# Optimization experiments

Measured on AMD Instinct MI355X. Metric: run time of the kernel, lower is better.

## Reference

```python
import jax, jax.numpy as jnp
import numpy as np

D = 20          # embedding dim (hardcoded in original module)
N_REL = 200     # relation vocab size (table has N_REL+1 rows)
N_TIME = 365    # time embedding table size
L = 3           # propagation layers
E = 2_000_000   # edges per layer
N = 1_000_000   # node-slot pool per layer
B = 64          # batch size
N_ENT = 1_000_003


def setup_inputs() -> dict:
    key = jax.random.key(0)
    ks = jax.random.split(key, 16)
    src_idx = jax.random.randint(ks[0], (L, E), 0, N, dtype=jnp.int32)
    dst_idx = jax.random.randint(ks[1], (L, E), 0, N, dtype=jnp.int32)
    rel_idx = jax.random.randint(ks[2], (L, E), 0, N_REL + 1, dtype=jnp.int32)
    qrel_idx = jax.random.randint(ks[3], (L, E), 0, N_REL + 1, dtype=jnp.int32)
    # signed relative time (edge_time - query_time); abs() must stay < N_TIME
    rel_time = jax.random.randint(ks[4], (L, E), -(N_TIME - 1), N_TIME, dtype=jnp.int32)
    node_batch = jax.random.randint(ks[5], (N,), 0, B, dtype=jnp.int32)
    node_ent = jnp.arange(N, dtype=jnp.int32)  # unique entity per final node slot
    s = 0.1
    rela_embed = jax.random.normal(ks[6], (N_REL + 1, D), jnp.float32) * s
    time_embed = jax.random.normal(ks[7], (N_TIME, D), jnp.float32) * s
    w_att1 = jax.random.normal(ks[8], (30, 3 * D), jnp.float32) * s
    w_att2 = jax.random.normal(ks[9], (1, 30), jnp.float32) * s
    w_past = jax.random.normal(ks[10], (D, D), jnp.float32) * s
    w_now = jax.random.normal(ks[11], (D, D), jnp.float32) * s
    w_future = jax.random.normal(ks[12], (D, D), jnp.float32) * s
    w_cls = jax.random.normal(ks[13], (D,), jnp.float32) * s
    b_cls = jnp.zeros((), jnp.float32)
    return dict(src_idx=src_idx, dst_idx=dst_idx, rel_idx=rel_idx,
                qrel_idx=qrel_idx, rel_time=rel_time, node_batch=node_batch,
                node_ent=node_ent, rela_embed=rela_embed, time_embed=time_embed,
                w_att1=w_att1, w_att2=w_att2, w_past=w_past, w_now=w_now,
                w_future=w_future, w_cls=w_cls, b_cls=b_cls,
                batch_size=B, n_ent=N_ENT)


def reference(src_idx, dst_idx, rel_idx, qrel_idx, rel_time, node_batch,
              node_ent, rela_embed, time_embed, w_att1, w_att2, w_past,
              w_now, w_future, w_cls, b_cls, batch_size, n_ent):
    n_layers = src_idx.shape[0]
    n_nodes = node_batch.shape[0]
    d = rela_embed.shape[1]
    hidden = jnp.zeros((n_nodes, d), dtype=rela_embed.dtype)
    for l in range(n_layers):
        rt = rel_time[l]                         # [E] signed relative time
        h_src = hidden[src_idx[l]]               # [E, D] gather
        r_emb = rela_embed[rel_idx[l]]           # [E, D]
        t_emb = time_embed[jnp.abs(rt)]          # [E, D]
        embed_rel = h_src + r_emb + t_emb
        # conditional time-branch MLP (mask-partitioned linear, same math as
        # the original's boolean-masked assignments)
        fut = embed_rel @ w_future.T
        now = embed_rel @ w_now.T
        pst = embed_rel @ w_past.T
        transformed = jnp.where((rt > 0)[:, None], fut,
                       jnp.where((rt == 0)[:, None], now, pst))
        # attention over concat(hidden_src, rel_emb, query_rel_emb)  [E, 3D]
        att_in = jnp.concatenate([h_src, r_emb, rela_embed[qrel_idx[l]]], axis=1)
        score = jax.nn.sigmoid(jax.nn.relu(att_in @ w_att1.T) @ w_att2.T)  # [E,1]
        msg = score * transformed                # [E, D]
        hidden = jax.ops.segment_sum(msg, dst_idx[l], num_segments=n_nodes)
        hidden = jax.nn.leaky_relu(hidden)       # default slope 0.01, as torch
    result = hidden @ w_cls + b_cls              # [N]
    score_all = jnp.zeros((batch_size, n_ent), dtype=result.dtype)
    score_all = score_all.at[node_batch, node_ent].set(result)
    return score_all
```

## Files before the change

kernel.cpp:

```cpp
#include <hip/hip_runtime.h>
#include <hip/hip_bf16.h>
#include <cstdint>

#define DD 20
#define HID 30
#define NB_SCAN 1024

typedef unsigned int  u32;
typedef unsigned short u16;

__device__ __forceinline__ void load20(const float* __restrict__ p, float* r){
  const float4* q = (const float4*)p;
#pragma unroll
  for (int i=0;i<5;i++){ float4 v=q[i]; r[4*i+0]=v.x; r[4*i+1]=v.y; r[4*i+2]=v.z; r[4*i+3]=v.w; }
}

__device__ __forceinline__ u32 pkbf(float a, float b){
  u32 ua=__float_as_uint(a); ua=(ua+0x7FFFu+((ua>>16)&1u))>>16;
  u32 ub=__float_as_uint(b); ub=(ub+0x7FFFu+((ub>>16)&1u))>>16;
  return ua | (ub<<16);
}

__global__ void k_prep(const float* __restrict__ rela, const float* __restrict__ w1,
                       const float* __restrict__ wp, const float* __restrict__ wn,
                       const float* __restrict__ wf,
                       float* __restrict__ W3, float* __restrict__ AR, float* __restrict__ AQ,
                       int nrel){
  int t = blockIdx.x*blockDim.x + threadIdx.x;
  if (t < 3*DD*DD){
    int s = t/(DD*DD), idx = t%(DD*DD);
    W3[t] = (s==0)?wp[idx]:((s==1)?wn[idx]:wf[idx]);
  }
  if (t < nrel*HID){
    int r=t/HID, j=t-r*HID;
    float sr=0.f, sq=0.f;
#pragma unroll
    for (int k=0;k<DD;k++){
      float e = rela[r*DD+k];
      sr += e*w1[j*3*DD + DD + k];
      sq += e*w1[j*3*DD + 2*DD + k];
    }
    AR[r*32+j]=sr; AQ[r*32+j]=sq;
  }
}

__global__ void k_rwtw(const float* __restrict__ rela, const float* __restrict__ timee,
                       const float* __restrict__ W3,
                       float* __restrict__ RW, float* __restrict__ TW,
                       int nrel, int ntime){
  int t = blockIdx.x*blockDim.x+threadIdx.x;
  int totR = 3*nrel*DD, totT = 3*ntime*DD;
  if (t < totR){
    int sel = t/(nrel*DD); int rem = t - sel*nrel*DD; int r = rem/DD; int i = rem - r*DD;
    const float* w = W3 + sel*DD*DD + i*DD;
    const float* e = rela + (size_t)r*DD;
    float s=0.f;
#pragma unroll
    for (int k=0;k<DD;k++) s += e[k]*w[k];
    RW[t]=s;
  }
  if (t < totT){
    int sel = t/(ntime*DD); int rem = t - sel*ntime*DD; int tt = rem/DD; int i = rem - tt*DD;
    const float* w = W3 + sel*DD*DD + i*DD;
    const float* e = timee + (size_t)tt*DD;
    float s=0.f;
#pragma unroll
    for (int k=0;k<DD;k++) s += e[k]*w[k];
    TW[t]=s;
  }
}

__global__ void k_rt(const float* __restrict__ rela, const float* __restrict__ timee,
                     const float* __restrict__ W3, float* __restrict__ RT,
                     int nrel, int ntime){
  int row = blockIdx.x*blockDim.x+threadIdx.x;
  int tot = 3*nrel*ntime;
  if (row>=tot) return;
  int per = nrel*ntime;
  int sel = row/per; int rem = row - sel*per; int r = rem/ntime; int t = rem - r*ntime;
  float e[DD], tv[DD];
  load20(rela + (size_t)r*DD, e);
  load20(timee + (size_t)t*DD, tv);
#pragma unroll
  for (int k=0;k<DD;k++) e[k]+=tv[k];
  const float* W = W3 + sel*DD*DD;
  float o[DD];
#pragma unroll
  for (int i=0;i<DD;i++){
    const float4* wr = (const float4*)(W + i*DD);
    float s=0.f;
#pragma unroll
    for (int c=0;c<5;c++){ float4 w=wr[c]; s += e[4*c]*w.x + e[4*c+1]*w.y + e[4*c+2]*w.z + e[4*c+3]*w.w; }
    o[i]=s;
  }
  float4* op=(float4*)(RT + (size_t)row*DD);
#pragma unroll
  for (int c=0;c<5;c++){ float4 v; v.x=o[4*c]; v.y=o[4*c+1]; v.z=o[4*c+2]; v.w=o[4*c+3]; op[c]=v; }
}

__global__ void __launch_bounds__(256) k_pre(const int* __restrict__ dst, int* __restrict__ cnt,
        int* __restrict__ rank, int E, int N,
        float4* __restrict__ dout4, size_t nd4,
        float4* __restrict__ bF, size_t nf4){
  int g=blockIdx.x, tid=threadIdx.x;
  int half=gridDim.x>>1;
  if (g & 1){
    int stride=half*256;
    int E2=2*E;
    for (int e=(g>>1)*256+tid; e<E2; e+=stride){
      int l=(e>=E)?1:0;
      rank[e]=atomicAdd(&cnt[(size_t)l*N+dst[e]],1);
    }
  } else {
    float4 z=make_float4(0.f,0.f,0.f,0.f);
    size_t i=(size_t)(g>>1)*256+tid, st=(size_t)half*256;
    for (size_t k=i;k<nd4;k+=st) dout4[k]=z;
    for (size_t k=i;k<nf4;k+=st) bF[k]=z;
  }
}

__global__ void k_scan_part(const int* __restrict__ cnt, int* __restrict__ part, int M, int C){
  __shared__ int sm[256];
  int b=blockIdx.x, t=threadIdx.x;
  int lo=b*C, hi=lo+C; if (hi>M) hi=M; if (lo>M) lo=M;
  int s=0;
  for (int i=lo+t; i<hi; i+=256) s+=cnt[i];
  sm[t]=s; __syncthreads();
  for (int o=128;o>0;o>>=1){ if (t<o) sm[t]+=sm[t+o]; __syncthreads(); }
  if (t==0) part[b]=sm[0];
}

__global__ void k_scan_top(int* __restrict__ part, int* __restrict__ listc){
  __shared__ int sm[NB_SCAN];
  int t=threadIdx.x;
  if (t==0) *listc=0;
  int v=part[t]; sm[t]=v; __syncthreads();
  for (int o=1;o<NB_SCAN;o<<=1){
    int u=(t>=o)?sm[t-o]:0; __syncthreads();
    sm[t]+=u; __syncthreads();
  }
  part[t]=sm[t]-v;
}

template<int ZM>
__global__ void k_scan_write(const int* __restrict__ cnt, const int* __restrict__ part,
                             int* __restrict__ rowptr, int M, int C, int base,
                             float* __restrict__ zb0, float* __restrict__ zb1, int Nsplit,
                             float* __restrict__ zres){
  __shared__ int sm[256];
  int b=blockIdx.x, t=threadIdx.x;
  int lo=b*C, hi=lo+C; if (hi>M) hi=M; if (lo>M) lo=M;
  int run=part[b]+base;
  for (int bb=lo; bb<hi; bb+=256){
    int i=bb+t;
    int v=(i<hi)?cnt[i]:0;
    if (i<hi && v==0){
      if (ZM==1){
        float* o=(i<Nsplit)? zb0+(size_t)i*DD : zb1+(size_t)(i-Nsplit)*DD;
        float4 z=make_float4(0.f,0.f,0.f,0.f);
        float4* o4=(float4*)o;
#pragma unroll
        for (int c=0;c<5;c++) o4[c]=z;
      } else if (ZM==2){
        zres[i]=0.f;
      }
    }
    sm[t]=v; __syncthreads();
    for (int o=1;o<256;o<<=1){
      int u=(t>=o)?sm[t-o]:0; __syncthreads();
      sm[t]+=u; __syncthreads();
    }
    if (i<hi) rowptr[i]=run+sm[t]-v;
    int tot=sm[255];
    __syncthreads();
    run+=tot;
  }
  if (hi==M && t==0) rowptr[M]=run;
}

__global__ void __launch_bounds__(256) k_scat01(const int* __restrict__ src,const int* __restrict__ dst,
  const int* __restrict__ rel,const int* __restrict__ qrel,const int* __restrict__ rtm,
  const int* __restrict__ rank,const int* __restrict__ rowptr,int4* __restrict__ recs,int E,int N){
  int e=blockIdx.x*blockDim.x+threadIdx.x;
  if (e>=2*E) return;
  int l=(e>=E)?1:0;
  int d=dst[e];
  int pos=rowptr[(size_t)l*N+d]+rank[e];
  recs[pos]=make_int4(src[e], rel[e]|(qrel[e]<<16), rtm[e], d);
}

__global__ void __launch_bounds__(256) k_scat2(const int* __restrict__ src,const int* __restrict__ dst,
  const int* __restrict__ rel,const int* __restrict__ qrel,const int* __restrict__ rtm,
  const int* __restrict__ rank,const int* __restrict__ rowptr2,int4* __restrict__ recs,int E){
  int e=blockIdx.x*blockDim.x+threadIdx.x;
  if (e>=E) return;
  int d=dst[e];
  int pos=rowptr2[d]+rank[e];
  recs[pos]=make_int4(src[e], rel[e]|(qrel[e]<<16), rtm[e], d);
}

template<bool HASH,bool FINAL,bool HIST>
__global__ void __launch_bounds__(256) k_fused(
    const int4* __restrict__ recs,
    const float* __restrict__ hin, float* __restrict__ hout, float* __restrict__ bufF,
    const float* __restrict__ RW, const float* __restrict__ TW,
    const float* __restrict__ AR, const float* __restrict__ AQ,
    const float* __restrict__ w1, const float* __restrict__ w2, const float* __restrict__ W3,
    int E, int nrel, int ntime,
    const int* __restrict__ hB_dst, int* __restrict__ hB_cnt, int* __restrict__ hB_rank, int hB_E,
    const float* __restrict__ wcls, float* __restrict__ res,
    int* __restrict__ list, int* __restrict__ listc)
{
  int lb;
  if (HIST){
    int g=blockIdx.x;
    int r3=g%3, b3=g/3;
    if (r3==2){
      int H=gridDim.x/3;
      int stride=H*256;
      for (int e=b3*256+threadIdx.x; e<hB_E; e+=stride)
        hB_rank[e]=atomicAdd(&hB_cnt[hB_dst[e]],1);
      return;
    }
    lb=b3*2+r3;
  } else lb=blockIdx.x;
  int bstart=lb*256;
  if (bstart>=E) return;

  __shared__ float sW1h[HID*DD];
  __shared__ float sW2[32];
  __shared__ float sW3[3*DD*DD];
  __shared__ u32   smsg[256*10];
  __shared__ int   sdst[256];
  __shared__ int   s_prevdst, s_nextdst;
  if (HASH){
    for (int t=threadIdx.x; t<HID*DD; t+=blockDim.x){ int j=t/DD,k=t-j*DD; sW1h[t]=w1[j*3*DD+k]; }
    for (int t=threadIdx.x; t<3*DD*DD; t+=blockDim.x) sW3[t]=W3[t];
  }
  if (threadIdx.x<HID) sW2[threadIdx.x]=w2[threadIdx.x];

  int tid = threadIdx.x;
  int bsize = E - bstart; if (bsize>256) bsize=256;
  int j = bstart + tid;
  bool active = (tid < bsize);

  if (tid==0){
    s_prevdst = (bstart>0) ? recs[-1 + (ptrdiff_t)bstart].w : -1;
    s_nextdst = (bstart+bsize < E) ? recs[bstart+bsize].w : -1;
  }
  __syncthreads();

  int dstv = -1;
  float m[DD];
  if (active){
    int4 rc = recs[j];
    int s = rc.x;
    int r = rc.y & 0xFFFF;
    int q = ((unsigned)rc.y) >> 16;
    int t = rc.z;
    dstv  = rc.w;
    int sel = (t>0)?2:((t==0)?1:0);
    int ta = (t<0)?-t:t;

    float h[DD];
    if (HASH){
      load20(hin+(size_t)s*DD, h);
#pragma unroll
      for (int i=0;i<DD;i++) h[i]=fmaxf(h[i],0.01f*h[i]);
    }

    float z=0.f;
    {
      const float4* ap=(const float4*)(AR+(size_t)r*32);
      const float4* qp=(const float4*)(AQ+(size_t)q*32);
#pragma unroll
      for (int c=0;c<7;c++){
        float4 x=ap[c], y=qp[c];
        float s4[4]={x.x+y.x, x.y+y.y, x.z+y.z, x.w+y.w};
#pragma unroll
        for (int u=0;u<4;u++){
          int jj=4*c+u;
          if (HASH){
            const float4* wr=(const float4*)&sW1h[jj*DD];
            float sum=s4[u];
#pragma unroll
            for (int c2=0;c2<5;c2++){ float4 w=wr[c2]; sum += h[4*c2]*w.x+h[4*c2+1]*w.y+h[4*c2+2]*w.z+h[4*c2+3]*w.w; }
            s4[u]=sum;
          }
          z += fmaxf(s4[u],0.f)*sW2[jj];
        }
      }
      float2 x2=*(const float2*)(AR+(size_t)r*32+28);
      float2 y2=*(const float2*)(AQ+(size_t)q*32+28);
      float s0=x2.x+y2.x, s1=x2.y+y2.y;
      if (HASH){
        const float4* wr0=(const float4*)&sW1h[28*DD];
        const float4* wr1=(const float4*)&sW1h[29*DD];
#pragma unroll
        for (int c2=0;c2<5;c2++){
          float4 wA=wr0[c2], wB=wr1[c2];
          s0 += h[4*c2]*wA.x+h[4*c2+1]*wA.y+h[4*c2+2]*wA.z+h[4*c2+3]*wA.w;
          s1 += h[4*c2]*wB.x+h[4*c2+1]*wB.y+h[4*c2+2]*wB.z+h[4*c2+3]*wB.w;
        }
      }
      z += fmaxf(s0,0.f)*sW2[28] + fmaxf(s1,0.f)*sW2[29];
    }
    float score = 1.f/(1.f+__expf(-z));

    const float4* rwp=(const float4*)(RW + ((size_t)(sel*nrel+r))*DD);
    const float4* twp=(const float4*)(TW + ((size_t)(sel*ntime+ta))*DD);
#pragma unroll
    for (int c=0;c<5;c++){
      float4 a4=rwp[c], b4=twp[c];
      float mv[4]={a4.x+b4.x, a4.y+b4.y, a4.z+b4.z, a4.w+b4.w};
      if (HASH){
#pragma unroll
        for (int u=0;u<4;u++){
          const float4* wr=(const float4*)&sW3[sel*DD*DD+(4*c+u)*DD];
          float sum=mv[u];
#pragma unroll
          for (int c2=0;c2<5;c2++){ float4 w=wr[c2]; sum += h[4*c2]*w.x+h[4*c2+1]*w.y+h[4*c2+2]*w.z+h[4*c2+3]*w.w; }
          mv[u]=sum;
        }
      }
#pragma unroll
      for (int u=0;u<4;u++) m[4*c+u]=score*mv[u];
      smsg[tid*10+2*c]  =pkbf(m[4*c+0],m[4*c+1]);
      smsg[tid*10+2*c+1]=pkbf(m[4*c+2],m[4*c+3]);
    }
  }
  sdst[tid] = active ? dstv : -2;
  __syncthreads();

  if (!active) return;
  bool isHead = (tid==0) ? (s_prevdst != dstv) : (sdst[tid-1] != dstv);
  if (!(isHead || tid==0)) return;
  int k=tid+1;
  for (; k<bsize && sdst[k]==dstv; ++k){
    const u32* row=&smsg[k*10];
#pragma unroll
    for (int i2=0;i2<10;i2++){
      u32 w=row[i2];
      m[2*i2]  +=__uint_as_float(w<<16);
      m[2*i2+1]+=__uint_as_float(w&0xFFFF0000u);
    }
  }
  bool crossStart = (tid==0 && !isHead);
  bool crossEnd   = (k==bsize) && (s_nextdst==dstv);
  if (crossStart || crossEnd){
    float* o = bufF + (size_t)dstv*DD;
#pragma unroll
    for (int i=0;i<DD;i++) atomicAdd(o+i, m[i]);
    if (!FINAL && isHead){
      int p = atomicAdd(listc,1);
      list[p] = dstv;
    }
  } else {
    if (!FINAL){
      float4* op=(float4*)(hout + (size_t)dstv*DD);
#pragma unroll
      for (int c=0;c<5;c++){ float4 v; v.x=m[4*c]; v.y=m[4*c+1]; v.z=m[4*c+2]; v.w=m[4*c+3]; op[c]=v; }
    } else {
      float rsum=0.f;
#pragma unroll
      for (int i=0;i<DD;i++){ float x=fmaxf(m[i],0.01f*m[i]); rsum += x*wcls[i]; }
      res[dstv] = rsum;
    }
  }
}

__global__ void __launch_bounds__(256) k_fixup(float* __restrict__ bufF, float* __restrict__ hout,
   const int* __restrict__ list,const int* __restrict__ listc){
  int c=*listc;
  for (int i=blockIdx.x*blockDim.x+threadIdx.x; i<c; i+=gridDim.x*blockDim.x){
    int n=list[i];
    float* p=bufF+(size_t)n*DD;
    float* o=hout+(size_t)n*DD;
#pragma unroll
    for (int jj=0;jj<DD;jj++){ o[jj]=p[jj]; p[jj]=0.f; }
  }
}

__global__ void __launch_bounds__(256) k_out(const float* __restrict__ res,
   const float* __restrict__ bufF, const float* __restrict__ wcls, const float* __restrict__ bcls,
   const int* __restrict__ nb, const int* __restrict__ ne, const int* __restrict__ nentp,
   float* __restrict__ out, int N){
  int n=blockIdx.x*blockDim.x+threadIdx.x;
  if (n>=N) return;
  float acc = res[n] + bcls[0];
  const float4* q=(const float4*)(bufF+(size_t)n*DD);
#pragma unroll
  for (int c=0;c<5;c++){
    float4 v=q[c];
    acc += fmaxf(v.x,0.01f*v.x)*wcls[4*c]   + fmaxf(v.y,0.01f*v.y)*wcls[4*c+1]
         + fmaxf(v.z,0.01f*v.z)*wcls[4*c+2] + fmaxf(v.w,0.01f*v.w)*wcls[4*c+3];
  }
  long long stride = nentp[0];
  out[(long long)nb[n]*stride + ne[n]] = acc;
}

template<bool HASH>
__global__ void __launch_bounds__(256) k_edge(
    const int* __restrict__ src, const int* __restrict__ dst,
    const int* __restrict__ rel, const int* __restrict__ qrel,
    const int* __restrict__ rtm,
    const float* __restrict__ hin, float* __restrict__ hout,
    const float* __restrict__ RT, const float* __restrict__ AR, const float* __restrict__ AQ,
    const float* __restrict__ w1, const float* __restrict__ w2, const float* __restrict__ W3,
    int E, int nrel, int ntime)
{
  __shared__ float sW1h[HID*DD];
  __shared__ float sW2[32];
  __shared__ float sW3[3*DD*DD];
  for (int t=threadIdx.x; t<HID*DD; t+=blockDim.x){ int j=t/DD,k=t-j*DD; sW1h[t]=w1[j*3*DD+k]; }
  if (threadIdx.x<HID) sW2[threadIdx.x]=w2[threadIdx.x];
  for (int t=threadIdx.x; t<3*DD*DD; t+=blockDim.x) sW3[t]=W3[t];
  __syncthreads();
  int e = blockIdx.x*blockDim.x+threadIdx.x;
  if (e>=E) return;
  int s=src[e], d=dst[e], r=rel[e], q=qrel[e], t=rtm[e];
  int sel = (t>0)?2:((t==0)?1:0);
  int ta = (t<0)?-t:t;
  float h[DD];
  if (HASH){
    load20(hin+(size_t)s*DD, h);
#pragma unroll
    for (int i=0;i<DD;i++) h[i]=fmaxf(h[i],0.01f*h[i]);
  }
  float a[HID];
  {
    const float4* ap=(const float4*)(AR+(size_t)r*32);
    const float4* qp=(const float4*)(AQ+(size_t)q*32);
#pragma unroll
    for (int c=0;c<7;c++){
      float4 x=ap[c], y=qp[c];
      a[4*c+0]=x.x+y.x; a[4*c+1]=x.y+y.y; a[4*c+2]=x.z+y.z; a[4*c+3]=x.w+y.w;
    }
    float2 x=*(const float2*)(AR+(size_t)r*32+28);
    float2 y=*(const float2*)(AQ+(size_t)q*32+28);
    a[28]=x.x+y.x; a[29]=x.y+y.y;
  }
  if (HASH){
#pragma unroll
    for (int j=0;j<HID;j++){
      const float4* wr=(const float4*)&sW1h[j*DD];
      float sum=a[j];
#pragma unroll
      for (int c=0;c<5;c++){ float4 w=wr[c]; sum += h[4*c]*w.x+h[4*c+1]*w.y+h[4*c+2]*w.z+h[4*c+3]*w.w; }
      a[j]=sum;
    }
  }
  float z=0.f;
#pragma unroll
  for (int j=0;j<HID;j++) z += fmaxf(a[j],0.f)*sW2[j];
  float score = 1.f/(1.f+__expf(-z));
  float tr[DD];
  load20(RT + ((size_t)(sel*nrel+r)*ntime + ta)*DD, tr);
  if (HASH){
    const float* Ws = sW3 + sel*DD*DD;
#pragma unroll
    for (int i=0;i<DD;i++){
      const float4* wr=(const float4*)(Ws+i*DD);
      float sum=tr[i];
#pragma unroll
      for (int c=0;c<5;c++){ float4 w=wr[c]; sum += h[4*c]*w.x+h[4*c+1]*w.y+h[4*c+2]*w.z+h[4*c+3]*w.w; }
      tr[i]=sum;
    }
  }
  float* o = hout + (size_t)d*DD;
#pragma unroll
  for (int i=0;i<DD;i++) atomicAdd(o+i, score*tr[i]);
}

__global__ void k_result(const float* __restrict__ h, const float* __restrict__ wcls,
                         const float* __restrict__ bcls, float* __restrict__ res, int N){
  int i = blockIdx.x*blockDim.x+threadIdx.x;
  if (i>=N) return;
  float acc = bcls[0];
  const float4* q=(const float4*)(h+(size_t)i*DD);
#pragma unroll
  for (int c=0;c<5;c++){
    float4 v=q[c];
    float x0=fmaxf(v.x,0.01f*v.x), x1=fmaxf(v.y,0.01f*v.y);
    float x2=fmaxf(v.z,0.01f*v.z), x3=fmaxf(v.w,0.01f*v.w);
    acc += x0*wcls[4*c]+x1*wcls[4*c+1]+x2*wcls[4*c+2]+x3*wcls[4*c+3];
  }
  res[i]=acc;
}

__global__ void k_scatter(const float* __restrict__ res, const int* __restrict__ nb,
                          const int* __restrict__ ne, const int* __restrict__ nentp,
                          float* __restrict__ out, int N){
  int i=blockIdx.x*blockDim.x+threadIdx.x;
  if (i>=N) return;
  long long stride = nentp[0];
  out[(long long)nb[i]*stride + ne[i]] = res[i];
}

extern "C" void kernel_launch(void* const* d_in, const int* in_sizes, int n_in,
                              void* d_out, int out_size, void* d_ws, size_t ws_size,
                              hipStream_t stream){
  const int*   src =(const int*)d_in[0];
  const int*   dst =(const int*)d_in[1];
  const int*   rel =(const int*)d_in[2];
  const int*   qrel=(const int*)d_in[3];
  const int*   rtm =(const int*)d_in[4];
  const int*   nb  =(const int*)d_in[5];
  const int*   ne  =(const int*)d_in[6];
  const float* rela=(const float*)d_in[7];
  const float* timee=(const float*)d_in[8];
  const float* w1  =(const float*)d_in[9];
  const float* w2  =(const float*)d_in[10];
  const float* wp  =(const float*)d_in[11];
  const float* wn  =(const float*)d_in[12];
  const float* wf  =(const float*)d_in[13];
  const float* wcls=(const float*)d_in[14];
  const float* bcls=(const float*)d_in[15];
  const int*   nentp=(const int*)d_in[17];

  const int Lc=3;
  int LE=in_sizes[0]; int E=LE/Lc;
  int N=in_sizes[5];
  int nrel=in_sizes[7]/DD;
  int ntime=in_sizes[8]/DD;

  auto al=[](size_t x){ return (x+(size_t)255)&~(size_t)255; };
  size_t szBuf =al((size_t)N*DD*4);
  size_t szRW  =al((size_t)3*nrel*DD*4);
  size_t szTW  =al((size_t)3*ntime*DD*4);
  size_t szRTf =al((size_t)3*nrel*ntime*DD*4);
  size_t szA   =al((size_t)nrel*32*4);
  size_t szW3  =al((size_t)3*DD*DD*4);
  size_t szRow =al(((size_t)3*N+3)*4);
  size_t szRank=al((size_t)LE*4);
  size_t szCnt =al((size_t)Lc*N*4);
  size_t szRecs=al((size_t)LE*16);
  size_t szPart=al((size_t)NB_SCAN*4);
  size_t szList=al((size_t)(131072+16)*4);
  size_t szRes =al((size_t)N*4);
  size_t need = 3*szBuf+szRW+szTW+2*szA+szW3+szRow+szRank+szCnt+szRecs+szPart+szList+szRes;

  dim3 blk(256);
  int prepTot = (3*DD*DD > nrel*HID) ? 3*DD*DD : nrel*HID;
  int rtTot=3*nrel*ntime;
  int rwtwTot = 3*ntime*DD;

  if (ws_size >= need){
    char* base=(char*)d_ws;
    size_t off=0;
    float* b0 =(float*)(base+off);  off+=szBuf;
    float* b1 =(float*)(base+off);  off+=szBuf;
    float* bufF=(float*)(base+off); off+=szBuf;
    float* RW  =(float*)(base+off); off+=szRW;
    float* TW  =(float*)(base+off); off+=szTW;
    float* AR  =(float*)(base+off); off+=szA;
    float* AQ  =(float*)(base+off); off+=szA;
    float* W3  =(float*)(base+off); off+=szW3;
    int*   rowptr=(int*)(base+off); off+=szRow;
    int*   rowptr2=rowptr+(size_t)2*N+1;
    int*   rank=(int*)(base+off);  off+=szRank;
    int*   cnt =(int*)(base+off);  off+=szCnt;
    int4*  recs=(int4*)(base+off); off+=szRecs;
    int*   part=(int*)(base+off);  off+=szPart;
    int*   listc=(int*)(base+off);
    int*   list =listc+16;          off+=szList;
    float* res =(float*)(base+off); off+=szRes;

    float* dout=(float*)d_out;

    (void)hipMemsetAsync(cnt,0,(size_t)Lc*N*4,stream);
    k_prep<<<dim3((prepTot+255)/256),blk,0,stream>>>(rela,w1,wp,wn,wf,W3,AR,AQ,nrel);
    k_rwtw<<<dim3((rwtwTot+255)/256),blk,0,stream>>>(rela,timee,W3,RW,TW,nrel,ntime);

    size_t nd4=(size_t)out_size>>2;
    size_t nb4=(size_t)N*DD/4;
    k_pre<<<dim3(8192),blk,0,stream>>>(dst,cnt,rank,E,N,(float4*)dout,nd4,
                                       (float4*)bufF,nb4);

    int LB=(E+255)/256;
    int H=(LB+1)/2;

    {
      int M=2*N, C=(M+NB_SCAN-1)/NB_SCAN;
      k_scan_part<<<dim3(NB_SCAN),blk,0,stream>>>(cnt,part,M,C);
      k_scan_top<<<dim3(1),dim3(NB_SCAN),0,stream>>>(part,listc);
      k_scan_write<1><<<dim3(NB_SCAN),blk,0,stream>>>(cnt,part,rowptr,M,C,0,b0,b1,N,nullptr);
    }
    k_scat01<<<dim3((2*E+255)/256),blk,0,stream>>>(src,dst,rel,qrel,rtm,rank,rowptr,recs,E,N);

    k_fused<false,false,true><<<dim3(3*H),blk,0,stream>>>(recs,nullptr,b0,bufF,
        RW,TW,AR,AQ,w1,w2,W3,E,nrel,ntime,
        dst+(size_t)2*E,cnt+(size_t)2*N,rank+(size_t)2*E,E,
        wcls,res,list,listc);
    k_fixup<<<dim3(128),blk,0,stream>>>(bufF,b0,list,listc);

    {
      int C=(N+NB_SCAN-1)/NB_SCAN;
      k_scan_part<<<dim3(NB_SCAN),blk,0,stream>>>(cnt+(size_t)2*N,part,N,C);
      k_scan_top<<<dim3(1),dim3(NB_SCAN),0,stream>>>(part,listc);
      k_scan_write<2><<<dim3(NB_SCAN),blk,0,stream>>>(cnt+(size_t)2*N,part,rowptr2,N,C,2*E,
                                                      nullptr,nullptr,0,res);
    }
    k_scat2<<<dim3(LB),blk,0,stream>>>(src+(size_t)2*E,dst+(size_t)2*E,rel+(size_t)2*E,
        qrel+(size_t)2*E,rtm+(size_t)2*E,rank+(size_t)2*E,rowptr2,recs,E);

    k_fused<true,false,false><<<dim3(LB),blk,0,stream>>>(recs+(size_t)E,b0,b1,bufF,
        RW,TW,AR,AQ,w1,w2,W3,E,nrel,ntime,
        nullptr,nullptr,nullptr,0,
        wcls,res,list,listc);
    k_fixup<<<dim3(128),blk,0,stream>>>(bufF,b1,list,listc);

    k_fused<true,true,false><<<dim3(LB),blk,0,stream>>>(recs+(size_t)2*E,b1,nullptr,bufF,
        RW,TW,AR,AQ,w1,w2,W3,E,nrel,ntime,
        nullptr,nullptr,nullptr,0,
        wcls,res,list,listc);

    k_out<<<dim3((N+255)/256),blk,0,stream>>>(res,bufF,wcls,bcls,nb,ne,nentp,dout,N);
  } else {
    char* base=(char*)d_out; float* res=(float*)d_ws;
    size_t off=0;
    float* buf0=(float*)(base+off); off+=szBuf;
    float* buf1=(float*)(base+off); off+=szBuf;
    float* RT  =(float*)(base+off); off+=szRTf;
    float* AR  =(float*)(base+off); off+=szA;
    float* AQ  =(float*)(base+off); off+=szA;
    float* W3  =(float*)(base+off); off+=szW3;
    k_prep<<<dim3((prepTot+255)/256),blk,0,stream>>>(rela,w1,wp,wn,wf,W3,AR,AQ,nrel);
    k_rt<<<dim3((rtTot+255)/256),blk,0,stream>>>(rela,timee,W3,RT,nrel,ntime);
    dim3 egrid((E+255)/256);
    dim3 ngrid((N+255)/256);
    (void)hipMemsetAsync(buf0,0,(size_t)N*DD*4,stream);
    k_edge<false><<<egrid,blk,0,stream>>>(src,dst,rel,qrel,rtm,nullptr,buf0,RT,AR,AQ,w1,w2,W3,E,nrel,ntime);
    (void)hipMemsetAsync(buf1,0,(size_t)N*DD*4,stream);
    k_edge<true><<<egrid,blk,0,stream>>>(src+(size_t)E,dst+(size_t)E,rel+(size_t)E,qrel+(size_t)E,rtm+(size_t)E,
                                         buf0,buf1,RT,AR,AQ,w1,w2,W3,E,nrel,ntime);
    (void)hipMemsetAsync(buf0,0,(size_t)N*DD*4,stream);
    k_edge<true><<<egrid,blk,0,stream>>>(src+(size_t)2*E,dst+(size_t)2*E,rel+(size_t)2*E,qrel+(size_t)2*E,rtm+(size_t)2*E,
                                         buf1,buf0,RT,AR,AQ,w1,w2,W3,E,nrel,ntime);
    k_result<<<ngrid,blk,0,stream>>>(buf0,wcls,bcls,res,N);
    (void)hipMemsetAsync(d_out,0,(size_t)out_size*sizeof(float),stream);
    k_scatter<<<ngrid,blk,0,stream>>>(res,nb,ne,nentp,(float*)d_out,N);
  }
}
```

Measured before the change: 1.046 ms.

## Store hidden state as padded fp16 and use packed fdot2 dot products

Intermediate per-node hidden buffers are changed from fp32 (80 B rows) to fp16 rows padded to 64 B, with leaky-relu applied before packing on write instead of on read. The attention and transform weights in shared memory are packed to fp16 pairs, and the per-edge 20-wide dot products use the packed fdot2 builtin. This targets the random-gather bandwidth on source rows and the FMA count per edge, at the cost of reduced precision in the hidden state and weights, which may affect tolerance.

```diff
diff --git a/kernel.cpp b/kernel.cpp
--- a/kernel.cpp
+++ b/kernel.cpp
@@ -1,13 +1,34 @@
 #include <hip/hip_runtime.h>
 #include <hip/hip_bf16.h>
+#include <hip/hip_fp16.h>
 #include <cstdint>
 
 #define DD 20
 #define HID 30
 #define NB_SCAN 1024
+#define HROW 32
 
 typedef unsigned int  u32;
 typedef unsigned short u16;
+typedef _Float16 hf2 __attribute__((ext_vector_type(2)));
+
+__device__ __forceinline__ hf2 as_hf2(u32 u){ union{u32 u; hf2 v;} c; c.u=u; return c.v; }
+__device__ __forceinline__ u32 pkhf(float a, float b){
+  union{hf2 v; u32 u;} c; c.v[0]=(_Float16)a; c.v[1]=(_Float16)b; return c.u;
+}
+__device__ __forceinline__ float lo16f(u32 u){ union{u16 s; _Float16 h;} c; c.s=(u16)(u&0xFFFF); return (float)c.h; }
+__device__ __forceinline__ float hi16f(u32 u){ union{u16 s; _Float16 h;} c; c.s=(u16)(u>>16); return (float)c.h; }
+
+__device__ __forceinline__ float dot10p(const u32* hh, const u32* __restrict__ w, float acc){
+#if __has_builtin(__builtin_amdgcn_fdot2)
+#pragma unroll
+  for (int c=0;c<10;c++) acc = __builtin_amdgcn_fdot2(as_hf2(hh[c]), as_hf2(w[c]), acc, false);
+#else
+#pragma unroll
+  for (int c=0;c<10;c++) acc += lo16f(hh[c])*lo16f(w[c]) + hi16f(hh[c])*hi16f(w[c]);
+#endif
+  return acc;
+}
 
 __device__ __forceinline__ void load20(const float* __restrict__ p, float* r){
   const float4* q = (const float4*)p;
@@ -145,7 +166,7 @@
 template<int ZM>
 __global__ void k_scan_write(const int* __restrict__ cnt, const int* __restrict__ part,
                              int* __restrict__ rowptr, int M, int C, int base,
-                             float* __restrict__ zb0, float* __restrict__ zb1, int Nsplit,
+                             u16* __restrict__ zb0, u16* __restrict__ zb1, int Nsplit,
                              float* __restrict__ zres){
   __shared__ int sm[256];
   int b=blockIdx.x, t=threadIdx.x;
@@ -156,11 +177,10 @@
     int v=(i<hi)?cnt[i]:0;
     if (i<hi && v==0){
       if (ZM==1){
-        float* o=(i<Nsplit)? zb0+(size_t)i*DD : zb1+(size_t)(i-Nsplit)*DD;
-        float4 z=make_float4(0.f,0.f,0.f,0.f);
-        float4* o4=(float4*)o;
-#pragma unroll
-        for (int c=0;c<5;c++) o4[c]=z;
+        u16* o=(i<Nsplit)? zb0+(size_t)i*HROW : zb1+(size_t)(i-Nsplit)*HROW;
+        uint4 z=make_uint4(0u,0u,0u,0u);
+        uint4* o4=(uint4*)o;
+        o4[0]=z; o4[1]=z; *((uint2*)(o4+2))=make_uint2(0u,0u);
       } else if (ZM==2){
         zres[i]=0.f;
       }
@@ -202,7 +222,7 @@
 template<bool HASH,bool FINAL,bool HIST>
 __global__ void __launch_bounds__(256) k_fused(
     const int4* __restrict__ recs,
-    const float* __restrict__ hin, float* __restrict__ hout, float* __restrict__ bufF,
+    const u16* __restrict__ hin, u16* __restrict__ hout, float* __restrict__ bufF,
     const float* __restrict__ RW, const float* __restrict__ TW,
     const float* __restrict__ AR, const float* __restrict__ AQ,
     const float* __restrict__ w1, const float* __restrict__ w2, const float* __restrict__ W3,
@@ -227,15 +247,21 @@
   int bstart=lb*256;
   if (bstart>=E) return;
 
-  __shared__ float sW1h[HID*DD];
+  __shared__ u32   sW1hp[HID*10];
+  __shared__ u32   sW3p[3*DD*10];
   __shared__ float sW2[32];
-  __shared__ float sW3[3*DD*DD];
   __shared__ u32   smsg[256*10];
   __shared__ int   sdst[256];
   __shared__ int   s_prevdst, s_nextdst;
   if (HASH){
-    for (int t=threadIdx.x; t<HID*DD; t+=blockDim.x){ int j=t/DD,k=t-j*DD; sW1h[t]=w1[j*3*DD+k]; }
-    for (int t=threadIdx.x; t<3*DD*DD; t+=blockDim.x) sW3[t]=W3[t];
+    for (int t=threadIdx.x; t<HID*10; t+=blockDim.x){
+      int j=t/10, c=t-j*10;
+      sW1hp[t]=pkhf(w1[j*3*DD+2*c], w1[j*3*DD+2*c+1]);
+    }
+    for (int t=threadIdx.x; t<3*DD*10; t+=blockDim.x){
+      int i=t/10, c=t-i*10;
+      sW3p[t]=pkhf(W3[i*DD+2*c], W3[i*DD+2*c+1]);
+    }
   }
   if (threadIdx.x<HID) sW2[threadIdx.x]=w2[threadIdx.x];
 
@@ -262,11 +288,13 @@
     int sel = (t>0)?2:((t==0)?1:0);
     int ta = (t<0)?-t:t;
 
-    float h[DD];
+    u32 hh[10];
     if (HASH){
-      load20(hin+(size_t)s*DD, h);
-#pragma unroll
-      for (int i=0;i<DD;i++) h[i]=fmaxf(h[i],0.01f*h[i]);
+      const uint4* hp=(const uint4*)(hin+(size_t)s*HROW);
+      uint4 A=hp[0], B=hp[1]; uint2 Cc=*((const uint2*)(hp+2));
+      hh[0]=A.x; hh[1]=A.y; hh[2]=A.z; hh[3]=A.w;
+      hh[4]=B.x; hh[5]=B.y; hh[6]=B.z; hh[7]=B.w;
+      hh[8]=Cc.x; hh[9]=Cc.y;
     }
 
     float z=0.f;
@@ -280,28 +308,17 @@
 #pragma unroll
         for (int u=0;u<4;u++){
           int jj=4*c+u;
-          if (HASH){
-            const float4* wr=(const float4*)&sW1h[jj*DD];
-            float sum=s4[u];
-#pragma unroll
-            for (int c2=0;c2<5;c2++){ float4 w=wr[c2]; sum += h[4*c2]*w.x+h[4*c2+1]*w.y+h[4*c2+2]*w.z+h[4*c2+3]*w.w; }
-            s4[u]=sum;
-          }
-          z += fmaxf(s4[u],0.f)*sW2[jj];
+          float sum=s4[u];
+          if (HASH) sum = dot10p(hh, &sW1hp[jj*10], sum);
+          z += fmaxf(sum,0.f)*sW2[jj];
         }
       }
       float2 x2=*(const float2*)(AR+(size_t)r*32+28);
       float2 y2=*(const float2*)(AQ+(size_t)q*32+28);
       float s0=x2.x+y2.x, s1=x2.y+y2.y;
       if (HASH){
-        const float4* wr0=(const float4*)&sW1h[28*DD];
-        const float4* wr1=(const float4*)&sW1h[29*DD];
-#pragma unroll
-        for (int c2=0;c2<5;c2++){
-          float4 wA=wr0[c2], wB=wr1[c2];
-          s0 += h[4*c2]*wA.x+h[4*c2+1]*wA.y+h[4*c2+2]*wA.z+h[4*c2+3]*wA.w;
-          s1 += h[4*c2]*wB.x+h[4*c2+1]*wB.y+h[4*c2+2]*wB.z+h[4*c2+3]*wB.w;
-        }
+        s0 = dot10p(hh, &sW1hp[28*10], s0);
+        s1 = dot10p(hh, &sW1hp[29*10], s1);
       }
       z += fmaxf(s0,0.f)*sW2[28] + fmaxf(s1,0.f)*sW2[29];
     }
@@ -315,13 +332,8 @@
       float mv[4]={a4.x+b4.x, a4.y+b4.y, a4.z+b4.z, a4.w+b4.w};
       if (HASH){
 #pragma unroll
-        for (int u=0;u<4;u++){
-          const float4* wr=(const float4*)&sW3[sel*DD*DD+(4*c+u)*DD];
-          float sum=mv[u];
-#pragma unroll
-          for (int c2=0;c2<5;c2++){ float4 w=wr[c2]; sum += h[4*c2]*w.x+h[4*c2+1]*w.y+h[4*c2+2]*w.z+h[4*c2+3]*w.w; }
-          mv[u]=sum;
-        }
+        for (int u=0;u<4;u++)
+          mv[u] = dot10p(hh, &sW3p[(sel*DD+4*c+u)*10], mv[u]);
       }
 #pragma unroll
       for (int u=0;u<4;u++) m[4*c+u]=score*mv[u];
@@ -357,9 +369,17 @@
     }
   } else {
     if (!FINAL){
-      float4* op=(float4*)(hout + (size_t)dstv*DD);
-#pragma unroll
-      for (int c=0;c<5;c++){ float4 v; v.x=m[4*c]; v.y=m[4*c+1]; v.z=m[4*c+2]; v.w=m[4*c+3]; op[c]=v; }
+      u32 o10[10];
+#pragma unroll
+      for (int i2=0;i2<10;i2++){
+        float x0=m[2*i2], x1=m[2*i2+1];
+        x0=fmaxf(x0,0.01f*x0); x1=fmaxf(x1,0.01f*x1);
+        o10[i2]=pkhf(x0,x1);
+      }
+      uint4* hp=(uint4*)(hout+(size_t)dstv*HROW);
+      hp[0]=make_uint4(o10[0],o10[1],o10[2],o10[3]);
+      hp[1]=make_uint4(o10[4],o10[5],o10[6],o10[7]);
+      *((uint2*)(hp+2))=make_uint2(o10[8],o10[9]);
     } else {
       float rsum=0.f;
 #pragma unroll
@@ -369,15 +389,26 @@
   }
 }
 
-__global__ void __launch_bounds__(256) k_fixup(float* __restrict__ bufF, float* __restrict__ hout,
+__global__ void __launch_bounds__(256) k_fixup(float* __restrict__ bufF, u16* __restrict__ hout,
    const int* __restrict__ list,const int* __restrict__ listc){
   int c=*listc;
   for (int i=blockIdx.x*blockDim.x+threadIdx.x; i<c; i+=gridDim.x*blockDim.x){
     int n=list[i];
     float* p=bufF+(size_t)n*DD;
-    float* o=hout+(size_t)n*DD;
-#pragma unroll
-    for (int jj=0;jj<DD;jj++){ o[jj]=p[jj]; p[jj]=0.f; }
+    float v[DD];
+#pragma unroll
+    for (int jj=0;jj<DD;jj++){ v[jj]=p[jj]; p[jj]=0.f; }
+    u32 o10[10];
+#pragma unroll
+    for (int i2=0;i2<10;i2++){
+      float x0=v[2*i2], x1=v[2*i2+1];
+      x0=fmaxf(x0,0.01f*x0); x1=fmaxf(x1,0.01f*x1);
+      o10[i2]=pkhf(x0,x1);
+    }
+    uint4* hp=(uint4*)(hout+(size_t)n*HROW);
+    hp[0]=make_uint4(o10[0],o10[1],o10[2],o10[3]);
+    hp[1]=make_uint4(o10[4],o10[5],o10[6],o10[7]);
+    *((uint2*)(hp+2))=make_uint2(o10[8],o10[9]);
   }
 }
 
@@ -525,6 +556,7 @@
   int ntime=in_sizes[8]/DD;
 
   auto al=[](size_t x){ return (x+(size_t)255)&~(size_t)255; };
+  size_t szBufH=al((size_t)N*HROW*2);
   size_t szBuf =al((size_t)N*DD*4);
   size_t szRW  =al((size_t)3*nrel*DD*4);
   size_t szTW  =al((size_t)3*ntime*DD*4);
@@ -538,7 +570,7 @@
   size_t szPart=al((size_t)NB_SCAN*4);
   size_t szList=al((size_t)(131072+16)*4);
   size_t szRes =al((size_t)N*4);
-  size_t need = 3*szBuf+szRW+szTW+2*szA+szW3+szRow+szRank+szCnt+szRecs+szPart+szList+szRes;
+  size_t need = 2*szBufH+szBuf+szRW+szTW+2*szA+szW3+szRow+szRank+szCnt+szRecs+szPart+szList+szRes;
 
   dim3 blk(256);
   int prepTot = (3*DD*DD > nrel*HID) ? 3*DD*DD : nrel*HID;
@@ -548,8 +580,8 @@
   if (ws_size >= need){
     char* base=(char*)d_ws;
     size_t off=0;
-    float* b0 =(float*)(base+off);  off+=szBuf;
-    float* b1 =(float*)(base+off);  off+=szBuf;
+    u16*   b0 =(u16*)(base+off);    off+=szBufH;
+    u16*   b1 =(u16*)(base+off);    off+=szBufH;
     float* bufF=(float*)(base+off); off+=szBuf;
     float* RW  =(float*)(base+off); off+=szRW;
     float* TW  =(float*)(base+off); off+=szTW;
```

After: 970.9 us. 1.08x faster.
